# Kernel optimization log

Hardware: AMD Instinct MI355X
Metric: run time of the kernel (lower is better)

Reference implementation:

```python
import jax, jax.numpy as jnp
import numpy as np

NUM_EXPERTS = 8
TOP_K = 2
IN_C, HID, OUT_C, R_C = 192, 384, 192, 8
B, H, W = 4, 128, 128


def setup_inputs() -> dict:
    key = jax.random.key(0)
    ks = jax.random.split(key, 12)
    s = 0.05
    return {
        "x": jax.random.normal(ks[0], (B, IN_C, H, W), jnp.float32),
        "router_input": jax.random.normal(ks[1], (B, R_C, H, W), jnp.float32),
        "router_W": jax.random.normal(ks[2], (NUM_EXPERTS, R_C), jnp.float32) * s,
        "router_b": jnp.zeros((NUM_EXPERTS,), jnp.float32),
        "W1": jax.random.normal(ks[3], (NUM_EXPERTS, HID, IN_C), jnp.float32) * s,
        "b1": jnp.zeros((NUM_EXPERTS, HID), jnp.float32),
        "W2": jax.random.normal(ks[4], (NUM_EXPERTS, HID, HID), jnp.float32) * s,
        "b2": jnp.zeros((NUM_EXPERTS, HID), jnp.float32),
        "W3": jax.random.normal(ks[5], (NUM_EXPERTS, OUT_C, HID), jnp.float32) * (s * 0.1),
        "b3": jnp.zeros((NUM_EXPERTS, OUT_C), jnp.float32),
    }


def _gates(router_input, router_W, router_b):
    # logits: (B, E, H, W) via 1x1 conv == per-pixel linear
    logits = jnp.einsum('ec,bchw->behw', router_W, router_input) + router_b[None, :, None, None]
    lt = jnp.moveaxis(logits, 1, -1)                      # (B,H,W,E)
    _, idx = jax.lax.top_k(lt, TOP_K)                     # (B,H,W,K)
    onehot = jax.nn.one_hot(idx, NUM_EXPERTS, dtype=bool).any(axis=-2)  # (B,H,W,E)
    masked = jnp.where(onehot, lt, -jnp.inf)
    gates = jax.nn.softmax(masked, axis=-1)               # (B,H,W,E)
    return jnp.moveaxis(gates, -1, 1)                     # (B,E,H,W)


def reference(x, router_input, router_W, router_b, W1, b1, W2, b2, W3, b3):
    gates = _gates(router_input, router_W, router_b)      # (B,E,H,W)
    out = jnp.zeros((x.shape[0], OUT_C) + x.shape[2:], x.dtype)
    gelu = lambda t: jax.nn.gelu(t, approximate=False)    # torch nn.GELU is exact
    for e in range(NUM_EXPERTS):
        h1 = gelu(jnp.einsum('oc,bchw->bohw', W1[e], x) + b1[e][None, :, None, None])
        h2 = gelu(jnp.einsum('oc,bchw->bohw', W2[e], h1) + b2[e][None, :, None, None])
        y = jnp.einsum('oc,bchw->bohw', W3[e], h2) + b3[e][None, :, None, None]
        out = out + gates[:, e:e + 1] * y
    return out
```

## Files before the change

kernel.cpp:

```cpp
#include <hip/hip_runtime.h>
#include <math.h>

#define NE 8
#define IN_C 192
#define HID 384
#define OUT_C 192
#define R_C 8
#define HW 16384
#define NPIX 65536
#define PPB 16384
#define TNP 64

typedef _Float16 h8_t __attribute__((ext_vector_type(8)));
typedef float f32x4 __attribute__((ext_vector_type(4)));

__device__ __forceinline__ float gelu_exact(float v) {
  float z  = v * 0.70710678118654752f;
  float az = fabsf(z);
  float t  = __builtin_amdgcn_rcpf(1.0f + 0.3275911f * az);
  float p  = ((((1.061405429f * t - 1.453152027f) * t + 1.421413741f) * t
               - 0.284496736f) * t + 0.254829592f) * t;
  float er = 1.0f - p * __expf(-z * z);
  er = copysignf(er, z);
  return 0.5f * v * (1.0f + er);
}

__device__ __forceinline__ void xt_block(const float* __restrict__ xb,
                                         _Float16* __restrict__ dst,
                                         int blk, int tid) {
  const int p = blk * 64 + (tid & 63);
  const int cq0 = tid >> 6;
#pragma unroll
  for (int cq = 0; cq < 6; ++cq) {
    int chq = cq * 4 + cq0;
    union { _Float16 h[8]; uint4 u; } pk;
#pragma unroll
    for (int j = 0; j < 8; ++j)
      pk.h[j] = (_Float16)xb[(size_t)(chq * 8 + j) * HW + p];
    *(uint4*)(dst + (size_t)p * 192 + chq * 8) = pk.u;
  }
}

__global__ __launch_bounds__(256) void prologue_kernel(
    const float* __restrict__ W1, const float* __restrict__ W2,
    const float* __restrict__ W3, _Float16* __restrict__ Wb,
    const float* __restrict__ rin, const float* __restrict__ rW,
    const float* __restrict__ rb, int* __restrict__ counts,
    int* __restrict__ lists, float* __restrict__ gatev,
    const float* __restrict__ x, _Float16* __restrict__ xt) {
  const int bid = blockIdx.x;
  const int tid = threadIdx.x;

  __shared__ int lcount[NE];
  __shared__ int lbase[NE];

  if (bid < 2304) {
    int t = bid * 256 + tid;
    if (t >= NE * 73728) return;
    int e = t / 73728, r = t % 73728;
    int cg = r / 1536, w = r % 1536;
    int j4 = w & 1, gm = w >> 1;
    int m = gm % 192, g = gm / 192;
    const float* src; int row, col, lda;
    if (cg < 6)       { src = W1 + (size_t)e * 73728;  row = m;       col = 32 * cg + 8 * g + 4 * j4; lda = 192; }
    else if (cg < 18) { int s = cg - 6;  int c = s >> 1, mh = s & 1;
                        src = W2 + (size_t)e * 147456; row = 192 * mh + m; col = 32 * c + 8 * g + 4 * j4; lda = 384; }
    else if (cg < 24) { int c = cg - 18;
                        src = W1 + (size_t)e * 73728;  row = 192 + m; col = 32 * c + 8 * g + 4 * j4; lda = 192; }
    else if (cg < 36) { int s = cg - 24; int c = s >> 1, mh = s & 1;
                        src = W2 + (size_t)e * 147456; row = 192 * mh + m; col = 192 + 32 * c + 8 * g + 4 * j4; lda = 384; }
    else              { int c = cg - 36;
                        src = W3 + (size_t)e * 73728;  row = m;       col = 32 * c + 8 * g + 4 * j4; lda = 384; }
    float4 v = *(const float4*)(src + (size_t)row * lda + col);
    union { _Float16 h4[4]; uint2 u; } cv;
    cv.h4[0] = (_Float16)v.x; cv.h4[1] = (_Float16)v.y;
    cv.h4[2] = (_Float16)v.z; cv.h4[3] = (_Float16)v.w;
    ((uint2*)Wb)[t] = cv.u;
  } else if (bid < 2560) {
    const int pid = (bid - 2304) * 256 + tid;
    const int img = pid >> 14;
    const int p = pid & (PPB - 1);

    if (tid < NE) lcount[tid] = 0;
    __syncthreads();

    const float* rbase = rin + (size_t)img * R_C * HW + p;
    float r[R_C];
#pragma unroll
    for (int c = 0; c < R_C; ++c) r[c] = rbase[(size_t)c * HW];
    float lg[NE];
#pragma unroll
    for (int e = 0; e < NE; ++e) {
      float s = rb[e];
#pragma unroll
      for (int c = 0; c < R_C; ++c) s += rW[e * R_C + c] * r[c];
      lg[e] = s;
    }
    int e0 = 0; float l0 = lg[0];
#pragma unroll
    for (int e = 1; e < NE; ++e) { if (lg[e] > l0) { l0 = lg[e]; e0 = e; } }
    int e1 = -1; float l1 = -3.4e38f;
#pragma unroll
    for (int e = 0; e < NE; ++e) {
      if (e != e0 && lg[e] > l1) { l1 = lg[e]; e1 = e; }
    }
    float ex  = expf(l1 - l0);
    float inv = 1.0f / (1.0f + ex);
    float g0 = inv, g1 = ex * inv;

    int pos0 = atomicAdd(&lcount[e0], 1);
    int pos1 = atomicAdd(&lcount[e1], 1);
    __syncthreads();
    if (tid < NE) lbase[tid] = atomicAdd(&counts[tid * 4 + img], lcount[tid]);
    __syncthreads();

    int i0 = (e0 * 4 + img) * PPB + lbase[e0] + pos0;
    lists[i0] = p;
    gatev[i0] = g0;
    int i1 = (e1 * 4 + img) * PPB + lbase[e1] + pos1;
    lists[i1] = p | (1 << 14);
    gatev[i1] = g1;
  } else {
    const int b2 = bid - 2560;
    const int img2 = b2 >> 8;
    xt_block(x + (size_t)img2 * IN_C * HW,
             xt + (size_t)img2 * PPB * 192, b2 & 255, tid);
  }
}

__device__ __forceinline__ void stage_chunk(const char* __restrict__ g,
                                            char* lds, int tid, int wid) {
  __builtin_amdgcn_global_load_lds(
      (const __attribute__((address_space(1))) void*)(g + tid * 16),
      (__attribute__((address_space(3))) void*)(lds + wid * 1024), 16, 0, 0);
  if (wid < 4)
    __builtin_amdgcn_global_load_lds(
        (const __attribute__((address_space(1))) void*)(g + 8192 + tid * 16),
        (__attribute__((address_space(3))) void*)(lds + 8192 + wid * 1024), 16, 0, 0);
}

__device__ __forceinline__ void pwait_c(int wid, bool last) {
  if (last)         asm volatile("s_waitcnt vmcnt(0)" ::: "memory");
  else if (wid < 4) asm volatile("s_waitcnt vmcnt(2)" ::: "memory");
  else              asm volatile("s_waitcnt vmcnt(1)" ::: "memory");
  __builtin_amdgcn_s_barrier();
  __builtin_amdgcn_sched_barrier(0);
}

__device__ __forceinline__ void read_B2(const _Float16* __restrict__ Bsh, int kb4,
                                        int nt0, int l15, int g, h8_t (&b)[2]) {
#pragma unroll
  for (int t = 0; t < 2; ++t)
    b[t] = *(const h8_t*)(Bsh + (((size_t)(kb4 + g) * TNP) + (nt0 + t) * 16 + l15) * 8);
}

__device__ __forceinline__ void mfma32(const _Float16* __restrict__ A, const h8_t (&b)[2],
                                       int m0, f32x4 (&acc)[3][2], int l15, int g) {
  h8_t a[3];
#pragma unroll
  for (int i = 0; i < 3; ++i)
    a[i] = *(const h8_t*)(A + ((size_t)g * 192 + m0 + i * 16 + l15) * 8);
  __builtin_amdgcn_s_setprio(1);
#pragma unroll
  for (int i = 0; i < 3; ++i)
#pragma unroll
    for (int t = 0; t < 2; ++t)
      acc[i][t] = __builtin_amdgcn_mfma_f32_16x16x32_f16(a[i], b[t], acc[i][t], 0, 0, 0);
  __builtin_amdgcn_s_setprio(0);
}

__device__ __forceinline__ void act_store(f32x4 (&acc)[3][2], const float* __restrict__ bias,
                                          _Float16* __restrict__ Dst, int m0, int nt0, int lane) {
  const int l15 = lane & 15, g = lane >> 4;
#pragma unroll
  for (int i = 0; i < 3; ++i) {
    int rb = m0 + i * 16 + 4 * g;
    float4 bv = *(const float4*)(bias + rb);
#pragma unroll
    for (int t = 0; t < 2; ++t) {
      int n = (nt0 + t) * 16 + l15;
      union { _Float16 h[4]; uint2 u; } cv;
      cv.h[0] = (_Float16)gelu_exact(acc[i][t][0] + bv.x);
      cv.h[1] = (_Float16)gelu_exact(acc[i][t][1] + bv.y);
      cv.h[2] = (_Float16)gelu_exact(acc[i][t][2] + bv.z);
      cv.h[3] = (_Float16)gelu_exact(acc[i][t][3] + bv.w);
      *(uint2*)(Dst + (((size_t)(rb >> 3) * TNP) + n) * 8 + (rb & 7)) = cv.u;
    }
  }
}

__device__ __forceinline__ void ybuf_store(f32x4 (&acc)[3][2], const float* __restrict__ bias,
                                           _Float16* __restrict__ ybuf,
                                           const int* __restrict__ pidsl,
                                           const float* __restrict__ pg,
                                           int npt, int m0, int nt0, int lane) {
  const int l15 = lane & 15, g = lane >> 4;
#pragma unroll
  for (int t = 0; t < 2; ++t) {
    int n = (nt0 + t) * 16 + l15;
    if (n >= npt) continue;
    float gt = pg[n];
    _Float16* yb = ybuf + pidsl[n];
#pragma unroll
    for (int i = 0; i < 3; ++i) {
      int rb = m0 + i * 16 + 4 * g;
      float4 bv = *(const float4*)(bias + rb);
      union { _Float16 h[4]; uint2 u; } cv;
      cv.h[0] = (_Float16)((acc[i][t][0] + bv.x) * gt);
      cv.h[1] = (_Float16)((acc[i][t][1] + bv.y) * gt);
      cv.h[2] = (_Float16)((acc[i][t][2] + bv.z) * gt);
      cv.h[3] = (_Float16)((acc[i][t][3] + bv.w) * gt);
      *(uint2*)(yb + rb) = cv.u;
    }
  }
}

__global__ __launch_bounds__(512, 4) void moe_mfma_kernel(
    const _Float16* __restrict__ xt, const _Float16* __restrict__ Wb,
    const float* __restrict__ b1, const float* __restrict__ b2,
    const float* __restrict__ b3,
    const int* __restrict__ counts, const int* __restrict__ lists,
    const float* __restrict__ gatev, _Float16* __restrict__ ybuf, int pair) {
  const int e = blockIdx.x;
  const int img2 = blockIdx.y >> 8;
  const int tile = blockIdx.y & 255;
  const int img = pair * 2 + img2;
  const int cnt = counts[e * 4 + img];
  const int start = tile * TNP;
  if (start >= cnt) return;
  const int npt = min(TNP, cnt - start);

  __shared__ __align__(16) char smem[78336];
  _Float16* XB  = (_Float16*)smem;
  _Float16* H1a = (_Float16*)(smem + 24576);
  _Float16* H2  = (_Float16*)smem;
  char* RING   = smem + 49152;
  float* BIAS1 = (float*)(smem + 73728);
  float* BIAS2 = (float*)(smem + 75264);
  float* BIAS3 = (float*)(smem + 76800);
  int*   pp    = (int*)(smem + 77568);
  int*   pidsl = (int*)(smem + 77824);
  float* pg    = (float*)(smem + 78080);

  const int tid = threadIdx.x;
  const int lane = tid & 63;
  const int wid = tid >> 6;
  const int l15 = lane & 15;
  const int g = lane >> 4;
  const int m0loc = (wid >> 1) * 48;
  const int nt0 = (wid & 1) * 2;

  if (tid < TNP) {
    int entry = 0; float gt = 0.0f;
    if (tid < npt) {
      entry = lists[(e * 4 + img) * PPB + start + tid];
      gt    = gatev[(e * 4 + img) * PPB + start + tid];
    }
    int p = entry & (PPB - 1);
    int slot = (entry >> 14) & 1;
    pp[tid] = img2 * PPB + p;
    pidsl[tid] = ((img2 * PPB + p) * 2 + slot) * 192;
    pg[tid] = gt;
  }
  for (int i = tid; i < 960; i += 512) {
    if (i < 384) BIAS1[i] = b1[e * HID + i];
    else if (i < 768) BIAS2[i - 384] = b2[e * HID + (i - 384)];
    else BIAS3[i - 768] = b3[e * OUT_C + (i - 768)];
  }
  __syncthreads();

  for (int i = tid; i < 24 * TNP; i += 512) {
    int n = i & (TNP - 1);
    int c16 = i >> 6;
    uint4 v = {0, 0, 0, 0};
    if (n < npt) v = *(const uint4*)(xt + (size_t)pp[n] * 192 + c16 * 8);
    *(uint4*)(XB + ((size_t)c16 * TNP + n) * 8) = v;
  }
  __syncthreads();

  const char* blob = (const char*)(Wb + (size_t)e * 294912);
  stage_chunk(blob, RING, tid, wid);
  stage_chunk(blob + 12288, RING + 12288, tid, wid);

  f32x4 acc1[3][2], acc2a[3][2], acc2b[3][2];
#pragma unroll
  for (int i = 0; i < 3; ++i)
#pragma unroll
    for (int t = 0; t < 2; ++t) {
      acc1[i][t] = (f32x4){0.f, 0.f, 0.f, 0.f};
      acc2a[i][t] = (f32x4){0.f, 0.f, 0.f, 0.f};
      acc2b[i][t] = (f32x4){0.f, 0.f, 0.f, 0.f};
    }

  h8_t b[2];

#pragma unroll
  for (int s = 0; s < 6; ++s) {
    pwait_c(wid, false);
    read_B2(XB, 4 * s, nt0, l15, g, b);
    mfma32((const _Float16*)(RING + (s & 1) * 12288), b, m0loc, acc1, l15, g);
    if (s == 5) {
      act_store(acc1, BIAS1, H1a, m0loc, nt0, lane);
      asm volatile("s_waitcnt lgkmcnt(0)");
    }
    __builtin_amdgcn_sched_barrier(0);
    __builtin_amdgcn_s_barrier();
    __builtin_amdgcn_sched_barrier(0);
    stage_chunk(blob + (size_t)(s + 2) * 12288, RING + (s & 1) * 12288, tid, wid);
  }

#pragma unroll
  for (int s = 0; s < 12; ++s) {
    pwait_c(wid, false);
    if ((s & 1) == 0) read_B2(H1a, 4 * (s >> 1), nt0, l15, g, b);
    mfma32((const _Float16*)(RING + (s & 1) * 12288), b, m0loc,
           (s & 1) ? acc2b : acc2a, l15, g);
    __builtin_amdgcn_sched_barrier(0);
    __builtin_amdgcn_s_barrier();
    __builtin_amdgcn_sched_barrier(0);
    stage_chunk(blob + (size_t)(s + 8) * 12288, RING + (s & 1) * 12288, tid, wid);
  }

#pragma unroll
  for (int i = 0; i < 3; ++i)
#pragma unroll
    for (int t = 0; t < 2; ++t) acc1[i][t] = (f32x4){0.f, 0.f, 0.f, 0.f};
#pragma unroll
  for (int s = 0; s < 6; ++s) {
    pwait_c(wid, false);
    read_B2(XB, 4 * s, nt0, l15, g, b);
    mfma32((const _Float16*)(RING + (s & 1) * 12288), b, m0loc, acc1, l15, g);
    if (s == 5) {
      act_store(acc1, BIAS1 + 192, H1a, m0loc, nt0, lane);
      asm volatile("s_waitcnt lgkmcnt(0)");
    }
    __builtin_amdgcn_sched_barrier(0);
    __builtin_amdgcn_s_barrier();
    __builtin_amdgcn_sched_barrier(0);
    stage_chunk(blob + (size_t)(s + 20) * 12288, RING + (s & 1) * 12288, tid, wid);
  }

#pragma unroll
  for (int s = 0; s < 12; ++s) {
    pwait_c(wid, false);
    if ((s & 1) == 0) read_B2(H1a, 4 * (s >> 1), nt0, l15, g, b);
    mfma32((const _Float16*)(RING + (s & 1) * 12288), b, m0loc,
           (s & 1) ? acc2b : acc2a, l15, g);
    if (s == 11) {
      act_store(acc2a, BIAS2, H2, m0loc, nt0, lane);
      act_store(acc2b, BIAS2, H2, 192 + m0loc, nt0, lane);
      asm volatile("s_waitcnt lgkmcnt(0)");
    }
    __builtin_amdgcn_sched_barrier(0);
    __builtin_amdgcn_s_barrier();
    __builtin_amdgcn_sched_barrier(0);
    stage_chunk(blob + (size_t)(s + 26) * 12288, RING + (s & 1) * 12288, tid, wid);
  }

#pragma unroll
  for (int i = 0; i < 3; ++i)
#pragma unroll
    for (int t = 0; t < 2; ++t) acc1[i][t] = (f32x4){0.f, 0.f, 0.f, 0.f};
#pragma unroll
  for (int s = 0; s < 12; ++s) {
    pwait_c(wid, s == 11);
    read_B2(H2, 4 * s, nt0, l15, g, b);
    mfma32((const _Float16*)(RING + (s & 1) * 12288), b, m0loc, acc1, l15, g);
    if (s < 10) {
      __builtin_amdgcn_sched_barrier(0);
      __builtin_amdgcn_s_barrier();
      __builtin_amdgcn_sched_barrier(0);
      stage_chunk(blob + (size_t)(s + 38) * 12288, RING + (s & 1) * 12288, tid, wid);
    }
  }

  ybuf_store(acc1, BIAS3, ybuf, pidsl, pg, npt, m0loc, nt0, lane);
}

__global__ __launch_bounds__(256) void sum_kernel(
    const _Float16* __restrict__ ybuf, float* __restrict__ out, int pair,
    const float* __restrict__ x, _Float16* __restrict__ xt, int xtp1) {
  __shared__ float ys[64][193];
  const int tid = threadIdx.x;

  if (xtp1 && blockIdx.x >= 512) {
    const int b2 = blockIdx.x - 512;
    const int img2 = b2 >> 8;
    xt_block(x + (size_t)(2 + img2) * IN_C * HW,
             xt + (size_t)img2 * PPB * 192, b2 & 255, tid);
    return;
  }

  const int img2 = blockIdx.x >> 8;
  const int p0 = (blockIdx.x & 255) * 64;
  const _Float16* yb = ybuf + (size_t)(img2 * PPB + p0) * 2 * 192;

  for (int t = tid; t < 64 * 48; t += 256) {
    int p = t / 48, c4 = t % 48;
    const uint2* y0 = (const uint2*)(yb + (size_t)p * 2 * 192) + c4;
    uint2 u0 = y0[0];
    uint2 u1 = y0[48];
    union { uint2 u; _Float16 h[4]; } a, b;
    a.u = u0; b.u = u1;
#pragma unroll
    for (int j = 0; j < 4; ++j)
      ys[p][c4 * 4 + j] = (float)a.h[j] + (float)b.h[j];
  }
  __syncthreads();

  float* ob = out + (size_t)(pair * 2 + img2) * OUT_C * HW + p0;
  for (int t = tid; t < OUT_C * 64; t += 256) {
    int c = t >> 6, p = t & 63;
    ob[(size_t)c * HW + p] = ys[p][c];
  }
}

extern "C" void kernel_launch(void* const* d_in, const int* in_sizes, int n_in,
                              void* d_out, int out_size, void* d_ws, size_t ws_size,
                              hipStream_t stream) {
  const float* x   = (const float*)d_in[0];
  const float* rin = (const float*)d_in[1];
  const float* rW  = (const float*)d_in[2];
  const float* rb  = (const float*)d_in[3];
  const float* W1  = (const float*)d_in[4];
  const float* b1  = (const float*)d_in[5];
  const float* W2  = (const float*)d_in[6];
  const float* b2  = (const float*)d_in[7];
  const float* W3  = (const float*)d_in[8];
  const float* b3  = (const float*)d_in[9];
  float* out = (float*)d_out;

  char* ws = (char*)d_ws;
  int*   counts = (int*)ws;
  int*   lists  = (int*)(ws + 1024);
  float* gatev  = (float*)(ws + 1024 + (size_t)NE * 4 * PPB * 4);
  _Float16* Wb  = (_Float16*)(ws + 1024 + 2 * (size_t)NE * 4 * PPB * 4);
  _Float16* ybuf = Wb + (size_t)NE * 294912;
  _Float16* xt = ybuf + (size_t)2 * PPB * 2 * 192;

  hipMemsetAsync(counts, 0, NE * 4 * sizeof(int), stream);

  prologue_kernel<<<3072, 256, 0, stream>>>(W1, W2, W3, Wb,
                                            rin, rW, rb, counts, lists, gatev,
                                            x, xt);

  moe_mfma_kernel<<<dim3(NE, 512), 512, 0, stream>>>(
      xt, Wb, b1, b2, b3, counts, lists, gatev, ybuf, 0);
  sum_kernel<<<1024, 256, 0, stream>>>(ybuf, out, 0, x, xt, 1);

  moe_mfma_kernel<<<dim3(NE, 512), 512, 0, stream>>>(
      xt, Wb, b1, b2, b3, counts, lists, gatev, ybuf, 1);
  sum_kernel<<<512, 256, 0, stream>>>(ybuf, out, 1, x, xt, 0);
}
```

Baseline: 233.7 us.

## Switch MoE GEMMs to 32x32x16 MFMA tiles with six-wave blocks

```diff
diff --git a/kernel.cpp b/kernel.cpp
--- a/kernel.cpp
+++ b/kernel.cpp
@@ -12,7 +12,7 @@
 #define TNP 64
 
 typedef _Float16 h8_t __attribute__((ext_vector_type(8)));
-typedef float f32x4 __attribute__((ext_vector_type(4)));
+typedef float f32x16 __attribute__((ext_vector_type(16)));
 
 __device__ __forceinline__ float gelu_exact(float v) {
   float z  = v * 0.70710678118654752f;
@@ -133,89 +133,84 @@
   __builtin_amdgcn_global_load_lds(
       (const __attribute__((address_space(1))) void*)(g + tid * 16),
       (__attribute__((address_space(3))) void*)(lds + wid * 1024), 16, 0, 0);
-  if (wid < 4)
-    __builtin_amdgcn_global_load_lds(
-        (const __attribute__((address_space(1))) void*)(g + 8192 + tid * 16),
-        (__attribute__((address_space(3))) void*)(lds + 8192 + wid * 1024), 16, 0, 0);
-}
-
-__device__ __forceinline__ void pwait_c(int wid, bool last) {
-  if (last)         asm volatile("s_waitcnt vmcnt(0)" ::: "memory");
-  else if (wid < 4) asm volatile("s_waitcnt vmcnt(2)" ::: "memory");
-  else              asm volatile("s_waitcnt vmcnt(1)" ::: "memory");
+  __builtin_amdgcn_global_load_lds(
+      (const __attribute__((address_space(1))) void*)(g + 6144 + tid * 16),
+      (__attribute__((address_space(3))) void*)(lds + 6144 + wid * 1024), 16, 0, 0);
+}
+
+__device__ __forceinline__ void pwait_u(bool last) {
+  if (last) asm volatile("s_waitcnt vmcnt(0)" ::: "memory");
+  else      asm volatile("s_waitcnt vmcnt(2)" ::: "memory");
   __builtin_amdgcn_s_barrier();
   __builtin_amdgcn_sched_barrier(0);
 }
 
-__device__ __forceinline__ void read_B2(const _Float16* __restrict__ Bsh, int kb4,
-                                        int nt0, int l15, int g, h8_t (&b)[2]) {
-#pragma unroll
-  for (int t = 0; t < 2; ++t)
-    b[t] = *(const h8_t*)(Bsh + (((size_t)(kb4 + g) * TNP) + (nt0 + t) * 16 + l15) * 8);
-}
-
-__device__ __forceinline__ void mfma32(const _Float16* __restrict__ A, const h8_t (&b)[2],
-                                       int m0, f32x4 (&acc)[3][2], int l15, int g) {
-  h8_t a[3];
-#pragma unroll
-  for (int i = 0; i < 3; ++i)
-    a[i] = *(const h8_t*)(A + ((size_t)g * 192 + m0 + i * 16 + l15) * 8);
+__device__ __forceinline__ void read_Bk(const _Float16* __restrict__ Bsh, int kb4,
+                                        int nt, int l31, int h, h8_t (&b)[2]) {
+  b[0] = *(const h8_t*)(Bsh + (((size_t)(kb4 + h) * TNP) + nt * 32 + l31) * 8);
+  b[1] = *(const h8_t*)(Bsh + (((size_t)(kb4 + 2 + h) * TNP) + nt * 32 + l31) * 8);
+}
+
+__device__ __forceinline__ void mfma_ph(const _Float16* __restrict__ A,
+                                        const h8_t (&b)[2], int mt0,
+                                        f32x16 (&acc)[2], int l31, int h) {
   __builtin_amdgcn_s_setprio(1);
 #pragma unroll
-  for (int i = 0; i < 3; ++i)
-#pragma unroll
-    for (int t = 0; t < 2; ++t)
-      acc[i][t] = __builtin_amdgcn_mfma_f32_16x16x32_f16(a[i], b[t], acc[i][t], 0, 0, 0);
+  for (int t = 0; t < 2; ++t) {
+    h8_t a0 = *(const h8_t*)(A + ((size_t)h * 192 + (mt0 + t) * 32 + l31) * 8);
+    acc[t] = __builtin_amdgcn_mfma_f32_32x32x16_f16(a0, b[0], acc[t], 0, 0, 0);
+    h8_t a1 = *(const h8_t*)(A + ((size_t)(2 + h) * 192 + (mt0 + t) * 32 + l31) * 8);
+    acc[t] = __builtin_amdgcn_mfma_f32_32x32x16_f16(a1, b[1], acc[t], 0, 0, 0);
+  }
   __builtin_amdgcn_s_setprio(0);
 }
 
-__device__ __forceinline__ void act_store(f32x4 (&acc)[3][2], const float* __restrict__ bias,
-                                          _Float16* __restrict__ Dst, int m0, int nt0, int lane) {
-  const int l15 = lane & 15, g = lane >> 4;
-#pragma unroll
-  for (int i = 0; i < 3; ++i) {
-    int rb = m0 + i * 16 + 4 * g;
-    float4 bv = *(const float4*)(bias + rb);
-#pragma unroll
-    for (int t = 0; t < 2; ++t) {
-      int n = (nt0 + t) * 16 + l15;
-      union { _Float16 h[4]; uint2 u; } cv;
-      cv.h[0] = (_Float16)gelu_exact(acc[i][t][0] + bv.x);
-      cv.h[1] = (_Float16)gelu_exact(acc[i][t][1] + bv.y);
-      cv.h[2] = (_Float16)gelu_exact(acc[i][t][2] + bv.z);
-      cv.h[3] = (_Float16)gelu_exact(acc[i][t][3] + bv.w);
+__device__ __forceinline__ void act_store32(f32x16 (&acc)[2], const float* __restrict__ bias,
+                                            _Float16* __restrict__ Dst, int mt0, int nt,
+                                            int l31, int h) {
+  const int n = nt * 32 + l31;
+#pragma unroll
+  for (int t = 0; t < 2; ++t) {
+#pragma unroll
+    for (int q = 0; q < 4; ++q) {
+      int rb = (mt0 + t) * 32 + q * 8 + 4 * h;
+      float4 bv = *(const float4*)(bias + rb);
+      union { _Float16 hh[4]; uint2 u; } cv;
+      cv.hh[0] = (_Float16)gelu_exact(acc[t][q * 4 + 0] + bv.x);
+      cv.hh[1] = (_Float16)gelu_exact(acc[t][q * 4 + 1] + bv.y);
+      cv.hh[2] = (_Float16)gelu_exact(acc[t][q * 4 + 2] + bv.z);
+      cv.hh[3] = (_Float16)gelu_exact(acc[t][q * 4 + 3] + bv.w);
       *(uint2*)(Dst + (((size_t)(rb >> 3) * TNP) + n) * 8 + (rb & 7)) = cv.u;
     }
   }
 }
 
-__device__ __forceinline__ void ybuf_store(f32x4 (&acc)[3][2], const float* __restrict__ bias,
-                                           _Float16* __restrict__ ybuf,
-                                           const int* __restrict__ pidsl,
-                                           const float* __restrict__ pg,
-                                           int npt, int m0, int nt0, int lane) {
-  const int l15 = lane & 15, g = lane >> 4;
+__device__ __forceinline__ void ybuf_store32(f32x16 (&acc)[2], const float* __restrict__ bias,
+                                             _Float16* __restrict__ ybuf,
+                                             const int* __restrict__ pidsl,
+                                             const float* __restrict__ pg,
+                                             int npt, int mt0, int nt, int l31, int h) {
+  const int n = nt * 32 + l31;
+  if (n >= npt) return;
+  float gt = pg[n];
+  _Float16* yb = ybuf + pidsl[n];
 #pragma unroll
   for (int t = 0; t < 2; ++t) {
-    int n = (nt0 + t) * 16 + l15;
-    if (n >= npt) continue;
-    float gt = pg[n];
-    _Float16* yb = ybuf + pidsl[n];
-#pragma unroll
-    for (int i = 0; i < 3; ++i) {
-      int rb = m0 + i * 16 + 4 * g;
+#pragma unroll
+    for (int q = 0; q < 4; ++q) {
+      int rb = (mt0 + t) * 32 + q * 8 + 4 * h;
       float4 bv = *(const float4*)(bias + rb);
-      union { _Float16 h[4]; uint2 u; } cv;
-      cv.h[0] = (_Float16)((acc[i][t][0] + bv.x) * gt);
-      cv.h[1] = (_Float16)((acc[i][t][1] + bv.y) * gt);
-      cv.h[2] = (_Float16)((acc[i][t][2] + bv.z) * gt);
-      cv.h[3] = (_Float16)((acc[i][t][3] + bv.w) * gt);
+      union { _Float16 hh[4]; uint2 u; } cv;
+      cv.hh[0] = (_Float16)((acc[t][q * 4 + 0] + bv.x) * gt);
+      cv.hh[1] = (_Float16)((acc[t][q * 4 + 1] + bv.y) * gt);
+      cv.hh[2] = (_Float16)((acc[t][q * 4 + 2] + bv.z) * gt);
+      cv.hh[3] = (_Float16)((acc[t][q * 4 + 3] + bv.w) * gt);
       *(uint2*)(yb + rb) = cv.u;
     }
   }
 }
 
-__global__ __launch_bounds__(512, 4) void moe_mfma_kernel(
+__global__ __launch_bounds__(384, 3) void moe_mfma_kernel(
     const _Float16* __restrict__ xt, const _Float16* __restrict__ Wb,
     const float* __restrict__ b1, const float* __restrict__ b2,
     const float* __restrict__ b3,
@@ -245,10 +240,10 @@
   const int tid = threadIdx.x;
   const int lane = tid & 63;
   const int wid = tid >> 6;
-  const int l15 = lane & 15;
-  const int g = lane >> 4;
-  const int m0loc = (wid >> 1) * 48;
-  const int nt0 = (wid & 1) * 2;
+  const int l31 = lane & 31;
+  const int h = lane >> 5;
+  const int mt0 = (wid >> 1) * 2;
+  const int nt = wid & 1;
 
   if (tid < TNP) {
     int entry = 0; float gt = 0.0f;
@@ -262,14 +257,14 @@
     pidsl[tid] = ((img2 * PPB + p) * 2 + slot) * 192;
     pg[tid] = gt;
   }
-  for (int i = tid; i < 960; i += 512) {
+  for (int i = tid; i < 960; i += 384) {
     if (i < 384) BIAS1[i] = b1[e * HID + i];
     else if (i < 768) BIAS2[i - 384] = b2[e * HID + (i - 384)];
     else BIAS3[i - 768] = b3[e * OUT_C + (i - 768)];
   }
   __syncthreads();
 
-  for (int i = tid; i < 24 * TNP; i += 512) {
+  for (int i = tid; i < 24 * TNP; i += 384) {
     int n = i & (TNP - 1);
     int c16 = i >> 6;
     uint4 v = {0, 0, 0, 0};
@@ -282,25 +277,24 @@
   stage_chunk(blob, RING, tid, wid);
   stage_chunk(blob + 12288, RING + 12288, tid, wid);
 
-  f32x4 acc1[3][2], acc2a[3][2], acc2b[3][2];
-#pragma unroll
-  for (int i = 0; i < 3; ++i)
-#pragma unroll
-    for (int t = 0; t < 2; ++t) {
-      acc1[i][t] = (f32x4){0.f, 0.f, 0.f, 0.f};
-      acc2a[i][t] = (f32x4){0.f, 0.f, 0.f, 0.f};
-      acc2b[i][t] = (f32x4){0.f, 0.f, 0.f, 0.f};
-    }
+  f32x16 acc1[2], acc2a[2], acc2b[2];
+#pragma unroll
+  for (int t = 0; t < 2; ++t) {
+#pragma unroll
+    for (int i = 0; i < 16; ++i) {
+      acc1[t][i] = 0.f; acc2a[t][i] = 0.f; acc2b[t][i] = 0.f;
+    }
+  }
 
   h8_t b[2];
 
 #pragma unroll
   for (int s = 0; s < 6; ++s) {
-    pwait_c(wid, false);
-    read_B2(XB, 4 * s, nt0, l15, g, b);
-    mfma32((const _Float16*)(RING + (s & 1) * 12288), b, m0loc, acc1, l15, g);
+    pwait_u(false);
+    read_Bk(XB, 4 * s, nt, l31, h, b);
+    mfma_ph((const _Float16*)(RING + (s & 1) * 12288), b, mt0, acc1, l31, h);
     if (s == 5) {
-      act_store(acc1, BIAS1, H1a, m0loc, nt0, lane);
+      act_store32(acc1, BIAS1, H1a, mt0, nt, l31, h);
       asm volatile("s_waitcnt lgkmcnt(0)");
     }
     __builtin_amdgcn_sched_barrier(0);
@@ -311,10 +305,10 @@
 
 #pragma unroll
   for (int s = 0; s < 12; ++s) {
-    pwait_c(wid, false);
-    if ((s & 1) == 0) read_B2(H1a, 4 * (s >> 1), nt0, l15, g, b);
-    mfma32((const _Float16*)(RING + (s & 1) * 12288), b, m0loc,
-           (s & 1) ? acc2b : acc2a, l15, g);
+    pwait_u(false);
+    if ((s & 1) == 0) read_Bk(H1a, 4 * (s >> 1), nt, l31, h, b);
+    mfma_ph((const _Float16*)(RING + (s & 1) * 12288), b, mt0,
+            (s & 1) ? acc2b : acc2a, l31, h);
     __builtin_amdgcn_sched_barrier(0);
     __builtin_amdgcn_s_barrier();
     __builtin_amdgcn_sched_barrier(0);
@@ -322,16 +316,16 @@
   }
 
 #pragma unroll
-  for (int i = 0; i < 3; ++i)
-#pragma unroll
-    for (int t = 0; t < 2; ++t) acc1[i][t] = (f32x4){0.f, 0.f, 0.f, 0.f};
+  for (int t = 0; t < 2; ++t)
+#pragma unroll
+    for (int i = 0; i < 16; ++i) acc1[t][i] = 0.f;
 #pragma unroll
   for (int s = 0; s < 6; ++s) {
-    pwait_c(wid, false);
-    read_B2(XB, 4 * s, nt0, l15, g, b);
-    mfma32((const _Float16*)(RING + (s & 1) * 12288), b, m0loc, acc1, l15, g);
+    pwait_u(false);
+    read_Bk(XB, 4 * s, nt, l31, h, b);
+    mfma_ph((const _Float16*)(RING + (s & 1) * 12288), b, mt0, acc1, l31, h);
     if (s == 5) {
-      act_store(acc1, BIAS1 + 192, H1a, m0loc, nt0, lane);
+      act_store32(acc1, BIAS1 + 192, H1a, mt0, nt, l31, h);
       asm volatile("s_waitcnt lgkmcnt(0)");
     }
     __builtin_amdgcn_sched_barrier(0);
@@ -342,13 +336,13 @@
 
 #pragma unroll
   for (int s = 0; s < 12; ++s) {
-    pwait_c(wid, false);
-    if ((s & 1) == 0) read_B2(H1a, 4 * (s >> 1), nt0, l15, g, b);
-    mfma32((const _Float16*)(RING + (s & 1) * 12288), b, m0loc,
-           (s & 1) ? acc2b : acc2a, l15, g);
+    pwait_u(false);
+    if ((s & 1) == 0) read_Bk(H1a, 4 * (s >> 1), nt, l31, h, b);
+    mfma_ph((const _Float16*)(RING + (s & 1) * 12288), b, mt0,
+            (s & 1) ? acc2b : acc2a, l31, h);
     if (s == 11) {
-      act_store(acc2a, BIAS2, H2, m0loc, nt0, lane);
-      act_store(acc2b, BIAS2, H2, 192 + m0loc, nt0, lane);
+      act_store32(acc2a, BIAS2, H2, mt0, nt, l31, h);
+      act_store32(acc2b, BIAS2, H2 + 192 * TNP * 8 / 8 * 0 + (size_t)24 * TNP * 8, mt0, nt, l31, h);
       asm volatile("s_waitcnt lgkmcnt(0)");
     }
     __builtin_amdgcn_sched_barrier(0);
@@ -358,14 +352,14 @@
   }
 
 #pragma unroll
-  for (int i = 0; i < 3; ++i)
-#pragma unroll
-    for (int t = 0; t < 2; ++t) acc1[i][t] = (f32x4){0.f, 0.f, 0.f, 0.f};
+  for (int t = 0; t < 2; ++t)
+#pragma unroll
+    for (int i = 0; i < 16; ++i) acc1[t][i] = 0.f;
 #pragma unroll
   for (int s = 0; s < 12; ++s) {
-    pwait_c(wid, s == 11);
-    read_B2(H2, 4 * s, nt0, l15, g, b);
-    mfma32((const _Float16*)(RING + (s & 1) * 12288), b, m0loc, acc1, l15, g);
+    pwait_u(s == 11);
+    read_Bk(H2, 4 * s, nt, l31, h, b);
+    mfma_ph((const _Float16*)(RING + (s & 1) * 12288), b, mt0, acc1, l31, h);
     if (s < 10) {
       __builtin_amdgcn_sched_barrier(0);
       __builtin_amdgcn_s_barrier();
@@ -374,7 +368,7 @@
     }
   }
 
-  ybuf_store(acc1, BIAS3, ybuf, pidsl, pg, npt, m0loc, nt0, lane);
+  ybuf_store32(acc1, BIAS3, ybuf, pidsl, pg, npt, mt0, nt, l31, h);
 }
 
 __global__ __launch_bounds__(256) void sum_kernel(
@@ -444,11 +438,11 @@
                                             rin, rW, rb, counts, lists, gatev,
                                             x, xt);
 
-  moe_mfma_kernel<<<dim3(NE, 512), 512, 0, stream>>>(
+  moe_mfma_kernel<<<dim3(NE, 512), 384, 0, stream>>>(
       xt, Wb, b1, b2, b3, counts, lists, gatev, ybuf, 0);
   sum_kernel<<<1024, 256, 0, stream>>>(ybuf, out, 0, x, xt, 1);
 
-  moe_mfma_kernel<<<dim3(NE, 512), 512, 0, stream>>>(
+  moe_mfma_kernel<<<dim3(NE, 512), 384, 0, stream>>>(
       xt, Wb, b1, b2, b3, counts, lists, gatev, ybuf, 1);
   sum_kernel<<<512, 256, 0, stream>>>(ybuf, out, 1, x, xt, 0);
 }
```

Result: slower. 313.4 us (+34.1%).
